# Performance work log

Hardware: AMD Instinct MI355X
Metric: run time of the kernel (lower is better)

## Reference

```python
import jax, jax.numpy as jnp
import numpy as np

B, V, E = 1024, 50257, 128

def setup_inputs() -> dict:
    key = jax.random.key(0)
    k1, k2, k3, k4 = jax.random.split(key, 4)
    # xs: one-hot focus-word vectors [B, V]
    focus_ids = jax.random.randint(k1, (B,), 0, V)
    xs = jnp.zeros((B, V), dtype=jnp.float32).at[jnp.arange(B), focus_ids].set(1.0)
    metric = jax.random.normal(k2, (E, E), dtype=jnp.float32)
    EMBEDM = jax.random.normal(k3, (V, E), dtype=jnp.float32)
    NEGEMBEDM = jax.random.normal(k4, (V, E), dtype=jnp.float32)
    return {"xs": xs, "metric": metric, "EMBEDM": EMBEDM, "NEGEMBEDM": NEGEMBEDM}

def reference(xs, metric, EMBEDM, NEGEMBEDM):
    # xs @ EMBEDM : one-hot matmul == row gather, but kept as GEMM to match original math
    xsembeds = xs @ EMBEDM                              # [B, E]
    # dots(vs, ws, metric) = (vs @ metric) @ ws.T
    scores = (xsembeds @ metric) @ NEGEMBEDM.T          # [B, V]
    return jax.nn.log_softmax(scores, axis=1)
```

## Files before the change

kernel.cpp:

```cpp
#include <hip/hip_runtime.h>
#include <hip/hip_bf16.h>
#include <math.h>

#define B_ROWS 1024
#define V_COLS 50257
#define E_DIM  128
#define BM     128
#define BN     128
#define NNB    393
#define VPAD   (NNB * BN)
#define N4     (V_COLS * E_DIM / 4)
#define N4P    (VPAD * E_DIM / 4)

typedef __attribute__((ext_vector_type(8))) short short8;
typedef __attribute__((ext_vector_type(4))) float floatx4;

static __device__ __forceinline__ unsigned short f2bf(float x) {
    union { float f; unsigned int u; } c; c.f = x;
    unsigned int u = c.u;
    unsigned int r = u + 0x7fffu + ((u >> 16) & 1u);
    return (unsigned short)(r >> 16);
}

static __device__ __forceinline__ void gload16(const void* g, void* l) {
    __builtin_amdgcn_global_load_lds(
        (const __attribute__((address_space(1))) void*)g,
        (__attribute__((address_space(3))) void*)l,
        16, 0, 0);
}

__global__ void find_idx_kernel(const float* __restrict__ xs, int* __restrict__ idx) {
    long i = (long)blockIdx.x * blockDim.x + threadIdx.x;
    const long n4 = (long)B_ROWS * V_COLS / 4;
    if (i >= n4) return;
    floatx4 v = __builtin_nontemporal_load((const floatx4*)xs + i);
    float vals[4] = {v.x, v.y, v.z, v.w};
    #pragma unroll
    for (int c = 0; c < 4; ++c) {
        if (vals[c] != 0.0f) {
            long f = 4 * i + c;
            int b = (int)(f / V_COLS);
            idx[b] = (int)(f - (long)b * V_COLS);
        }
    }
}

__global__ void cvt_bf16_kernel(const float* __restrict__ src, ushort4* __restrict__ dst) {
    int i = blockIdx.x * blockDim.x + threadIdx.x;
    if (i >= N4P) return;
    ushort4 o;
    if (i < N4) {
        floatx4 v = __builtin_nontemporal_load((const floatx4*)src + i);
        o.x = f2bf(v.x); o.y = f2bf(v.y); o.z = f2bf(v.z); o.w = f2bf(v.w);
    } else {
        o.x = 0; o.y = 0; o.z = 0; o.w = 0;
    }
    dst[i] = o;
}

__global__ void compute_t_kernel(const float* __restrict__ EMB, const float* __restrict__ metric,
                                 const int* __restrict__ idx, unsigned short* __restrict__ t) {
    __shared__ float erow[E_DIM];
    int b = blockIdx.x, tid = threadIdx.x;
    int id = idx[b];
    erow[tid] = EMB[(long)id * E_DIM + tid];
    __syncthreads();
    float acc = 0.f;
    #pragma unroll 16
    for (int k = 0; k < E_DIM; ++k) acc += erow[k] * metric[k * E_DIM + tid];
    t[b * E_DIM + tid] = f2bf(acc);
}

template <bool WRITE_OUT>
__global__ __launch_bounds__(512, 4) void gemm_kernel(const unsigned short* __restrict__ t,
                                                      const unsigned short* __restrict__ neg,
                                                      float2* __restrict__ partials,
                                                      const float* __restrict__ lse,
                                                      float* __restrict__ out) {
    __shared__ __align__(16) unsigned char smem[128 * 132 * 4];
    __shared__ float2 stats[4][128];
    __shared__ float lsev[128];

    const int tid  = threadIdx.x;
    const int lane = tid & 63, wave = tid >> 6;
    const int l16  = lane & 15, q = lane >> 4;
    const int wm   = wave >> 2, wn = wave & 3;
    const int mbase = blockIdx.x * BM;
    const int nbase = blockIdx.y * BN;

    if (WRITE_OUT && tid < 128) lsev[tid] = lse[mbase + tid];

    uint4* ldsA = (uint4*)smem;
    uint4* ldsB = (uint4*)(smem + 32768);
    const uint4* srcA = (const uint4*)(t + (size_t)mbase * E_DIM);
    const uint4* srcB = (const uint4*)(neg + (size_t)nbase * E_DIM);
    {
        const int p0 = wave * 256 + lane;
        #pragma unroll
        for (int i = 0; i < 4; ++i) {
            int p = p0 + i * 64;
            int r = p >> 4, c = p & 15;
            int s = (r << 4) + (c ^ (r & 15));
            int pbase = wave * 256 + i * 64;
            gload16(srcA + s, ldsA + pbase);
            gload16(srcB + s, ldsB + pbase);
        }
    }
    __syncthreads();

    floatx4 acc[4][2];
    #pragma unroll
    for (int i = 0; i < 4; ++i)
        #pragma unroll
        for (int j = 0; j < 2; ++j) acc[i][j] = (floatx4){0, 0, 0, 0};

    #pragma unroll
    for (int ks = 0; ks < 4; ++ks) {
        short8 af[4], bfr[2];
        #pragma unroll
        for (int mf = 0; mf < 4; ++mf) {
            int row = wm * 64 + mf * 16 + l16;
            af[mf] = *(const short8*)&ldsA[(row << 4) + ((ks * 4 + q) ^ (row & 15))];
        }
        #pragma unroll
        for (int nf = 0; nf < 2; ++nf) {
            int row = wn * 32 + nf * 16 + l16;
            bfr[nf] = *(const short8*)&ldsB[(row << 4) + ((ks * 4 + q) ^ (row & 15))];
        }
        #pragma unroll
        for (int mf = 0; mf < 4; ++mf)
            #pragma unroll
            for (int nf = 0; nf < 2; ++nf)
                acc[mf][nf] = __builtin_amdgcn_mfma_f32_16x16x32_bf16(af[mf], bfr[nf], acc[mf][nf], 0, 0, 0);
    }


    if (!WRITE_OUT) {
        const bool v0 = (nbase + wn * 32 + l16) < V_COLS;
        const bool v1 = (nbase + wn * 32 + 16 + l16) < V_COLS;
        #pragma unroll
        for (int mf = 0; mf < 4; ++mf) {
            #pragma unroll
            for (int r = 0; r < 4; ++r) {
                float mx = -INFINITY;
                if (v0) mx = acc[mf][0][r];
                if (v1) mx = fmaxf(mx, acc[mf][1][r]);
                #pragma unroll
                for (int d = 1; d < 16; d <<= 1) mx = fmaxf(mx, __shfl_xor(mx, d, 16));
                float s = 0.f;
                if (v0) s += __expf(acc[mf][0][r] - mx);
                if (v1) s += __expf(acc[mf][1][r] - mx);
                #pragma unroll
                for (int d = 1; d < 16; d <<= 1) s += __shfl_xor(s, d, 16);
                if (l16 == 0) stats[wn][wm * 64 + mf * 16 + q * 4 + r] = make_float2(mx, s);
            }
        }
        __syncthreads();
        if (tid < 128) {
            float2 p0 = stats[0][tid], p1 = stats[1][tid], p2 = stats[2][tid], p3 = stats[3][tid];
            float mm = fmaxf(fmaxf(p0.x, p1.x), fmaxf(p2.x, p3.x));
            float ss = p0.y * __expf(p0.x - mm) + p1.y * __expf(p1.x - mm)
                     + p2.y * __expf(p2.x - mm) + p3.y * __expf(p3.x - mm);
            partials[(long)(mbase + tid) * NNB + blockIdx.y] = make_float2(mm, ss);
        }
    } else {
        __syncthreads();
        float* sbuf = (float*)smem;
        #pragma unroll
        for (int mf = 0; mf < 4; ++mf)
            #pragma unroll
            for (int nf = 0; nf < 2; ++nf)
                #pragma unroll
                for (int r = 0; r < 4; ++r)
                    sbuf[(wm * 64 + mf * 16 + q * 4 + r) * 132 + wn * 32 + nf * 16 + l16] = acc[mf][nf][r];
        __syncthreads();
        #pragma unroll 4
        for (int it = 0; it < 32; ++it) {
            int i = it * 512 + tid;
            int r = i >> 7, c = i & 127;
            int col = nbase + c;
            if (col < V_COLS)
                __builtin_nontemporal_store(sbuf[r * 132 + c] - lsev[r],
                                            &out[(size_t)(mbase + r) * V_COLS + col]);
        }
    }
}

__global__ void merge_lse_kernel(const float2* __restrict__ partials, float* __restrict__ lse) {
    int b = blockIdx.x;
    int tid = threadIdx.x;
    float m = -INFINITY, s = 0.f;
    for (int i = tid; i < NNB; i += 256) {
        float2 p = partials[(long)b * NNB + i];
        if (p.x > m) { s = s * __expf(m - p.x) + p.y; m = p.x; }
        else         { s += p.y * __expf(p.x - m); }
    }
    __shared__ float sm[256], ss[256];
    sm[tid] = m; ss[tid] = s;
    __syncthreads();
    for (int off = 128; off > 0; off >>= 1) {
        if (tid < off) {
            float m1 = sm[tid], s1 = ss[tid];
            float m2 = sm[tid + off], s2 = ss[tid + off];
            float mm = fmaxf(m1, m2);
            sm[tid] = mm;
            ss[tid] = s1 * __expf(m1 - mm) + s2 * __expf(m2 - mm);
        }
        __syncthreads();
    }
    if (tid == 0) lse[b] = sm[0] + __logf(ss[0]);
}

extern "C" void kernel_launch(void* const* d_in, const int* in_sizes, int n_in,
                              void* d_out, int out_size, void* d_ws, size_t ws_size,
                              hipStream_t stream) {
    const float* xs     = (const float*)d_in[0];
    const float* metric = (const float*)d_in[1];
    const float* EMB    = (const float*)d_in[2];
    const float* NEG    = (const float*)d_in[3];
    float* out = (float*)d_out;

    char* ws = (char*)d_ws;
    int*            idx      = (int*)ws;
    unsigned short* t        = (unsigned short*)(ws + 4096);
    unsigned short* neg16    = (unsigned short*)(ws + 266240);
    float2*         partials = (float2*)(ws + 13144064);
    float*          lse      = (float*)(ws + 16363520);

    {
        long n4 = (long)B_ROWS * V_COLS / 4;
        int blocks = (int)((n4 + 255) / 256);
        find_idx_kernel<<<blocks, 256, 0, stream>>>(xs, idx);
    }
    cvt_bf16_kernel<<<(N4P + 255) / 256, 256, 0, stream>>>(NEG, (ushort4*)neg16);
    compute_t_kernel<<<B_ROWS, E_DIM, 0, stream>>>(EMB, metric, idx, t);
    gemm_kernel<false><<<dim3(B_ROWS / BM, NNB), 512, 0, stream>>>(t, neg16, partials, nullptr, nullptr);
    merge_lse_kernel<<<B_ROWS, 256, 0, stream>>>(partials, lse);
    gemm_kernel<true><<<dim3(B_ROWS / BM, NNB), 512, 0, stream>>>(t, neg16, partials, lse, out);
}
```

Before: 474.2 us.

## Fuse GEMM passes into one score write with an in-place LSE subtract

Replaces the two-pass GEMM (one pass for softmax stats, one recomputing scores to write the normalized output) with a single pass. That pass writes raw scores to the output and emits per-tile max/sum partials. A new merge kernel combines the partials into the row log-sum-exp and subtracts it in place from the output using vectorized read-modify-write. This removes the recomputed GEMM and a launch. In exchange, the full B×V output is read and written a second time, and the nontemporal store hint is dropped.

```diff
diff --git a/kernel.cpp b/kernel.cpp
--- a/kernel.cpp
+++ b/kernel.cpp
@@ -71,15 +71,12 @@
     t[b * E_DIM + tid] = f2bf(acc);
 }
 
-template <bool WRITE_OUT>
-__global__ __launch_bounds__(512, 4) void gemm_kernel(const unsigned short* __restrict__ t,
-                                                      const unsigned short* __restrict__ neg,
-                                                      float2* __restrict__ partials,
-                                                      const float* __restrict__ lse,
-                                                      float* __restrict__ out) {
+__global__ __launch_bounds__(512, 4) void gemm_score_kernel(const unsigned short* __restrict__ t,
+                                                            const unsigned short* __restrict__ neg,
+                                                            float2* __restrict__ partials,
+                                                            float* __restrict__ out) {
     __shared__ __align__(16) unsigned char smem[128 * 132 * 4];
     __shared__ float2 stats[4][128];
-    __shared__ float lsev[128];
 
     const int tid  = threadIdx.x;
     const int lane = tid & 63, wave = tid >> 6;
@@ -87,8 +84,6 @@
     const int wm   = wave >> 2, wn = wave & 3;
     const int mbase = blockIdx.x * BM;
     const int nbase = blockIdx.y * BN;
-
-    if (WRITE_OUT && tid < 128) lsev[tid] = lse[mbase + tid];
 
     uint4* ldsA = (uint4*)smem;
     uint4* ldsB = (uint4*)(smem + 32768);
@@ -135,70 +130,68 @@
     }
 
 
-    if (!WRITE_OUT) {
-        const bool v0 = (nbase + wn * 32 + l16) < V_COLS;
-        const bool v1 = (nbase + wn * 32 + 16 + l16) < V_COLS;
-        #pragma unroll
-        for (int mf = 0; mf < 4; ++mf) {
-            #pragma unroll
-            for (int r = 0; r < 4; ++r) {
-                float mx = -INFINITY;
-                if (v0) mx = acc[mf][0][r];
-                if (v1) mx = fmaxf(mx, acc[mf][1][r]);
-                #pragma unroll
-                for (int d = 1; d < 16; d <<= 1) mx = fmaxf(mx, __shfl_xor(mx, d, 16));
-                float s = 0.f;
-                if (v0) s += __expf(acc[mf][0][r] - mx);
-                if (v1) s += __expf(acc[mf][1][r] - mx);
-                #pragma unroll
-                for (int d = 1; d < 16; d <<= 1) s += __shfl_xor(s, d, 16);
-                if (l16 == 0) stats[wn][wm * 64 + mf * 16 + q * 4 + r] = make_float2(mx, s);
-            }
-        }
-        __syncthreads();
-        if (tid < 128) {
-            float2 p0 = stats[0][tid], p1 = stats[1][tid], p2 = stats[2][tid], p3 = stats[3][tid];
-            float mm = fmaxf(fmaxf(p0.x, p1.x), fmaxf(p2.x, p3.x));
-            float ss = p0.y * __expf(p0.x - mm) + p1.y * __expf(p1.x - mm)
-                     + p2.y * __expf(p2.x - mm) + p3.y * __expf(p3.x - mm);
-            partials[(long)(mbase + tid) * NNB + blockIdx.y] = make_float2(mm, ss);
-        }
-    } else {
-        __syncthreads();
-        float* sbuf = (float*)smem;
-        #pragma unroll
-        for (int mf = 0; mf < 4; ++mf)
-            #pragma unroll
-            for (int nf = 0; nf < 2; ++nf)
-                #pragma unroll
-                for (int r = 0; r < 4; ++r)
-                    sbuf[(wm * 64 + mf * 16 + q * 4 + r) * 132 + wn * 32 + nf * 16 + l16] = acc[mf][nf][r];
-        __syncthreads();
-        #pragma unroll 4
-        for (int it = 0; it < 32; ++it) {
-            int i = it * 512 + tid;
-            int r = i >> 7, c = i & 127;
-            int col = nbase + c;
-            if (col < V_COLS)
-                __builtin_nontemporal_store(sbuf[r * 132 + c] - lsev[r],
-                                            &out[(size_t)(mbase + r) * V_COLS + col]);
-        }
-    }
-}
-
-__global__ void merge_lse_kernel(const float2* __restrict__ partials, float* __restrict__ lse) {
+    const bool v0 = (nbase + wn * 32 + l16) < V_COLS;
+    const bool v1 = (nbase + wn * 32 + 16 + l16) < V_COLS;
+    #pragma unroll
+    for (int mf = 0; mf < 4; ++mf) {
+        #pragma unroll
+        for (int r = 0; r < 4; ++r) {
+            float mx = -INFINITY;
+            if (v0) mx = acc[mf][0][r];
+            if (v1) mx = fmaxf(mx, acc[mf][1][r]);
+            #pragma unroll
+            for (int d = 1; d < 16; d <<= 1) mx = fmaxf(mx, __shfl_xor(mx, d, 16));
+            float s = 0.f;
+            if (v0) s += __expf(acc[mf][0][r] - mx);
+            if (v1) s += __expf(acc[mf][1][r] - mx);
+            #pragma unroll
+            for (int d = 1; d < 16; d <<= 1) s += __shfl_xor(s, d, 16);
+            if (l16 == 0) stats[wn][wm * 64 + mf * 16 + q * 4 + r] = make_float2(mx, s);
+        }
+    }
+    __syncthreads();
+
+    if (tid < 128) {
+        float2 p0 = stats[0][tid], p1 = stats[1][tid], p2 = stats[2][tid], p3 = stats[3][tid];
+        float mm = fmaxf(fmaxf(p0.x, p1.x), fmaxf(p2.x, p3.x));
+        float ss = p0.y * __expf(p0.x - mm) + p1.y * __expf(p1.x - mm)
+                 + p2.y * __expf(p2.x - mm) + p3.y * __expf(p3.x - mm);
+        partials[(long)(mbase + tid) * NNB + blockIdx.y] = make_float2(mm, ss);
+    }
+
+    float* sbuf = (float*)smem;
+    #pragma unroll
+    for (int mf = 0; mf < 4; ++mf)
+        #pragma unroll
+        for (int nf = 0; nf < 2; ++nf)
+            #pragma unroll
+            for (int r = 0; r < 4; ++r)
+                sbuf[(wm * 64 + mf * 16 + q * 4 + r) * 132 + wn * 32 + nf * 16 + l16] = acc[mf][nf][r];
+    __syncthreads();
+    #pragma unroll 4
+    for (int it = 0; it < 32; ++it) {
+        int i = it * 512 + tid;
+        int r = i >> 7, c = i & 127;
+        int col = nbase + c;
+        if (col < V_COLS)
+            out[(size_t)(mbase + r) * V_COLS + col] = sbuf[r * 132 + c];
+    }
+}
+
+__global__ __launch_bounds__(512) void merge_sub_kernel(const float2* __restrict__ partials,
+                                                        float* __restrict__ out) {
     int b = blockIdx.x;
     int tid = threadIdx.x;
     float m = -INFINITY, s = 0.f;
-    for (int i = tid; i < NNB; i += 256) {
+    for (int i = tid; i < NNB; i += 512) {
         float2 p = partials[(long)b * NNB + i];
         if (p.x > m) { s = s * __expf(m - p.x) + p.y; m = p.x; }
         else         { s += p.y * __expf(p.x - m); }
     }
-    __shared__ float sm[256], ss[256];
+    __shared__ float sm[512], ss[512];
     sm[tid] = m; ss[tid] = s;
     __syncthreads();
-    for (int off = 128; off > 0; off >>= 1) {
+    for (int off = 256; off > 0; off >>= 1) {
         if (tid < off) {
             float m1 = sm[tid], s1 = ss[tid];
             float m2 = sm[tid + off], s2 = ss[tid + off];
@@ -208,7 +201,24 @@
         }
         __syncthreads();
     }
-    if (tid == 0) lse[b] = sm[0] + __logf(ss[0]);
+    __shared__ float lse_sh;
+    if (tid == 0) lse_sh = sm[0] + __logf(ss[0]);
+    __syncthreads();
+    const float l = lse_sh;
+
+    float* p = out + (size_t)b * V_COLS;
+    int mis  = (int)(((unsigned long long)(uintptr_t)p >> 2) & 3ull);
+    int head = (4 - mis) & 3;
+    if (tid < head) p[tid] -= l;
+    int n4 = (V_COLS - head) >> 2;
+    floatx4* p4 = (floatx4*)(p + head);
+    for (int i = tid; i < n4; i += 512) {
+        floatx4 v = p4[i];
+        v -= l;
+        p4[i] = v;
+    }
+    int done = head + (n4 << 2);
+    if (tid < V_COLS - done) p[done + tid] -= l;
 }
 
 extern "C" void kernel_launch(void* const* d_in, const int* in_sizes, int n_in,
@@ -225,7 +235,6 @@
     unsigned short* t        = (unsigned short*)(ws + 4096);
     unsigned short* neg16    = (unsigned short*)(ws + 266240);
     float2*         partials = (float2*)(ws + 13144064);
-    float*          lse      = (float*)(ws + 16363520);
 
     {
         long n4 = (long)B_ROWS * V_COLS / 4;
@@ -234,7 +243,6 @@
     }
     cvt_bf16_kernel<<<(N4P + 255) / 256, 256, 0, stream>>>(NEG, (ushort4*)neg16);
     compute_t_kernel<<<B_ROWS, E_DIM, 0, stream>>>(EMB, metric, idx, t);
-    gemm_kernel<false><<<dim3(B_ROWS / BM, NNB), 512, 0, stream>>>(t, neg16, partials, nullptr, nullptr);
-    merge_lse_kernel<<<B_ROWS, 256, 0, stream>>>(partials, lse);
-    gemm_kernel<true><<<dim3(B_ROWS / BM, NNB), 512, 0, stream>>>(t, neg16, partials, lse, out);
-}
+    gemm_score_kernel<<<dim3(B_ROWS / BM, NNB), 512, 0, stream>>>(t, neg16, partials, out);
+    merge_sub_kernel<<<B_ROWS, 512, 0, stream>>>(partials, out);
+}
```

Result: faster. 456.0 us (-3.8%).

## Make GEMM persistent over vocab chunks with double-buffered B tiles and online softmax

Applied to the files above, without the earlier changes.

The one-tile-per-block GEMM grid is replaced by 256 blocks, each owning a 128-row M tile and a contiguous chunk of about 12 vocab tiles. The A fragment stays in registers and B tiles are double-buffered in LDS with async global-to-LDS loads. The stats pass now keeps running max/sum per row in registers, and merge_lse shrinks to one 128-thread wave reduction. The write pass stores directly from registers instead of staging through LDS, which risks less-coalesced output stores and lower occupancy with only 256 blocks.

```diff
diff --git a/kernel.cpp b/kernel.cpp
--- a/kernel.cpp
+++ b/kernel.cpp
@@ -11,6 +11,7 @@
 #define VPAD   (NNB * BN)
 #define N4     (V_COLS * E_DIM / 4)
 #define N4P    (VPAD * E_DIM / 4)
+#define NCHUNK 32
 
 typedef __attribute__((ext_vector_type(8))) short short8;
 typedef __attribute__((ext_vector_type(4))) float floatx4;
@@ -72,143 +73,161 @@
 }
 
 template <bool WRITE_OUT>
-__global__ __launch_bounds__(512, 4) void gemm_kernel(const unsigned short* __restrict__ t,
-                                                      const unsigned short* __restrict__ neg,
-                                                      float2* __restrict__ partials,
-                                                      const float* __restrict__ lse,
-                                                      float* __restrict__ out) {
-    __shared__ __align__(16) unsigned char smem[128 * 132 * 4];
-    __shared__ float2 stats[4][128];
-    __shared__ float lsev[128];
+__global__ __launch_bounds__(512, 2) void gemm_chunk_kernel(const unsigned short* __restrict__ t,
+                                                            const unsigned short* __restrict__ neg,
+                                                            float2* __restrict__ partials,
+                                                            const float* __restrict__ lse,
+                                                            float* __restrict__ out) {
+    __shared__ __align__(16) uint4 bbuf[2][2048];
+
+    const int lin  = blockIdx.x;
+    const int m    = (lin >> 3) & 7;
+    const int c    = (lin & 7) | ((lin >> 6) << 3);
+    const int t0   = (c * NNB) / NCHUNK;
+    const int t1   = ((c + 1) * NNB) / NCHUNK;
 
     const int tid  = threadIdx.x;
     const int lane = tid & 63, wave = tid >> 6;
     const int l16  = lane & 15, q = lane >> 4;
     const int wm   = wave >> 2, wn = wave & 3;
-    const int mbase = blockIdx.x * BM;
-    const int nbase = blockIdx.y * BN;
-
-    if (WRITE_OUT && tid < 128) lsev[tid] = lse[mbase + tid];
-
-    uint4* ldsA = (uint4*)smem;
-    uint4* ldsB = (uint4*)(smem + 32768);
-    const uint4* srcA = (const uint4*)(t + (size_t)mbase * E_DIM);
-    const uint4* srcB = (const uint4*)(neg + (size_t)nbase * E_DIM);
-    {
-        const int p0 = wave * 256 + lane;
+    const int mbase = m * BM;
+
+    short8 af[4][4];
+    #pragma unroll
+    for (int mf = 0; mf < 4; ++mf)
+        #pragma unroll
+        for (int ks = 0; ks < 4; ++ks)
+            af[mf][ks] = *(const short8*)&t[(size_t)(mbase + wm * 64 + mf * 16 + l16) * E_DIM + ks * 32 + q * 8];
+
+    float lsev[4][4];
+    float mrun[4][4], srun[4][4];
+    if (WRITE_OUT) {
+        #pragma unroll
+        for (int mf = 0; mf < 4; ++mf)
+            #pragma unroll
+            for (int r = 0; r < 4; ++r)
+                lsev[mf][r] = lse[mbase + wm * 64 + mf * 16 + q * 4 + r];
+    } else {
+        #pragma unroll
+        for (int mf = 0; mf < 4; ++mf)
+            #pragma unroll
+            for (int r = 0; r < 4; ++r) { mrun[mf][r] = -INFINITY; srun[mf][r] = 0.f; }
+    }
+
+    const int p0 = wave * 256 + lane;
+    auto STAGE = [&](int buf, int tile) {
+        const uint4* srcB = (const uint4*)(neg + (size_t)tile * BN * E_DIM);
         #pragma unroll
         for (int i = 0; i < 4; ++i) {
             int p = p0 + i * 64;
-            int r = p >> 4, c = p & 15;
-            int s = (r << 4) + (c ^ (r & 15));
-            int pbase = wave * 256 + i * 64;
-            gload16(srcA + s, ldsA + pbase);
-            gload16(srcB + s, ldsB + pbase);
-        }
-    }
+            int r = p >> 4, cc = p & 15;
+            int s = (r << 4) + (cc ^ (r & 15));
+            gload16(srcB + s, &bbuf[buf][wave * 256 + i * 64]);
+        }
+    };
+
+    STAGE(0, t0);
     __syncthreads();
 
-    floatx4 acc[4][2];
+    for (int tt = t0; tt < t1; ++tt) {
+        const int cur = (tt - t0) & 1;
+        if (tt + 1 < t1) STAGE(cur ^ 1, tt + 1);
+
+        floatx4 acc[4][2];
+        #pragma unroll
+        for (int i = 0; i < 4; ++i)
+            #pragma unroll
+            for (int j = 0; j < 2; ++j) acc[i][j] = (floatx4){0, 0, 0, 0};
+
+        #pragma unroll
+        for (int ks = 0; ks < 4; ++ks) {
+            short8 bfr[2];
+            #pragma unroll
+            for (int nf = 0; nf < 2; ++nf) {
+                int row = wn * 32 + nf * 16 + l16;
+                bfr[nf] = *(const short8*)&bbuf[cur][(row << 4) + ((ks * 4 + q) ^ (row & 15))];
+            }
+            #pragma unroll
+            for (int mf = 0; mf < 4; ++mf)
+                #pragma unroll
+                for (int nf = 0; nf < 2; ++nf)
+                    acc[mf][nf] = __builtin_amdgcn_mfma_f32_16x16x32_bf16(af[mf][ks], bfr[nf], acc[mf][nf], 0, 0, 0);
+        }
+
+        const int col0 = tt * BN + wn * 32 + l16;
+        const bool v0 = col0 < V_COLS;
+        const bool v1 = (col0 + 16) < V_COLS;
+
+        if (!WRITE_OUT) {
+            #pragma unroll
+            for (int mf = 0; mf < 4; ++mf)
+                #pragma unroll
+                for (int r = 0; r < 4; ++r) {
+                    float a0 = v0 ? acc[mf][0][r] : -INFINITY;
+                    float a1 = v1 ? acc[mf][1][r] : -INFINITY;
+                    float nm = fmaxf(mrun[mf][r], fmaxf(a0, a1));
+                    float s  = srun[mf][r] * __expf(mrun[mf][r] - nm);
+                    if (v0) s += __expf(a0 - nm);
+                    if (v1) s += __expf(a1 - nm);
+                    mrun[mf][r] = nm; srun[mf][r] = s;
+                }
+        } else {
+            #pragma unroll
+            for (int mf = 0; mf < 4; ++mf) {
+                const size_t rowb = (size_t)(mbase + wm * 64 + mf * 16 + q * 4) * V_COLS;
+                #pragma unroll
+                for (int r = 0; r < 4; ++r) {
+                    if (v0) out[rowb + (size_t)r * V_COLS + col0]      = acc[mf][0][r] - lsev[mf][r];
+                    if (v1) out[rowb + (size_t)r * V_COLS + col0 + 16] = acc[mf][1][r] - lsev[mf][r];
+                }
+            }
+        }
+        __syncthreads();
+    }
+
+    if (!WRITE_OUT) {
+        #pragma unroll
+        for (int mf = 0; mf < 4; ++mf)
+            #pragma unroll
+            for (int r = 0; r < 4; ++r) {
+                float mm = mrun[mf][r], ss = srun[mf][r];
+                #pragma unroll
+                for (int d = 1; d < 16; d <<= 1) {
+                    float mo = __shfl_xor(mm, d, 16);
+                    float so = __shfl_xor(ss, d, 16);
+                    float nm = fmaxf(mm, mo);
+                    ss = ss * __expf(mm - nm) + so * __expf(mo - nm);
+                    mm = nm;
+                }
+                if (l16 == 0) {
+                    int row_local = wm * 64 + mf * 16 + q * 4 + r;
+                    partials[(((size_t)mbase + row_local) * NCHUNK + c) * 4 + wn] = make_float2(mm, ss);
+                }
+            }
+    }
+}
+
+__global__ __launch_bounds__(128) void merge_lse_kernel(const float2* __restrict__ partials,
+                                                        float* __restrict__ lse) {
+    int b = blockIdx.x, tid = threadIdx.x;
+    float2 p = partials[(size_t)b * 128 + tid];
+    float mm = p.x, ss = p.y;
     #pragma unroll
-    for (int i = 0; i < 4; ++i)
-        #pragma unroll
-        for (int j = 0; j < 2; ++j) acc[i][j] = (floatx4){0, 0, 0, 0};
-
-    #pragma unroll
-    for (int ks = 0; ks < 4; ++ks) {
-        short8 af[4], bfr[2];
-        #pragma unroll
-        for (int mf = 0; mf < 4; ++mf) {
-            int row = wm * 64 + mf * 16 + l16;
-            af[mf] = *(const short8*)&ldsA[(row << 4) + ((ks * 4 + q) ^ (row & 15))];
-        }
-        #pragma unroll
-        for (int nf = 0; nf < 2; ++nf) {
-            int row = wn * 32 + nf * 16 + l16;
-            bfr[nf] = *(const short8*)&ldsB[(row << 4) + ((ks * 4 + q) ^ (row & 15))];
-        }
-        #pragma unroll
-        for (int mf = 0; mf < 4; ++mf)
-            #pragma unroll
-            for (int nf = 0; nf < 2; ++nf)
-                acc[mf][nf] = __builtin_amdgcn_mfma_f32_16x16x32_bf16(af[mf], bfr[nf], acc[mf][nf], 0, 0, 0);
-    }
-
-
-    if (!WRITE_OUT) {
-        const bool v0 = (nbase + wn * 32 + l16) < V_COLS;
-        const bool v1 = (nbase + wn * 32 + 16 + l16) < V_COLS;
-        #pragma unroll
-        for (int mf = 0; mf < 4; ++mf) {
-            #pragma unroll
-            for (int r = 0; r < 4; ++r) {
-                float mx = -INFINITY;
-                if (v0) mx = acc[mf][0][r];
-                if (v1) mx = fmaxf(mx, acc[mf][1][r]);
-                #pragma unroll
-                for (int d = 1; d < 16; d <<= 1) mx = fmaxf(mx, __shfl_xor(mx, d, 16));
-                float s = 0.f;
-                if (v0) s += __expf(acc[mf][0][r] - mx);
-                if (v1) s += __expf(acc[mf][1][r] - mx);
-                #pragma unroll
-                for (int d = 1; d < 16; d <<= 1) s += __shfl_xor(s, d, 16);
-                if (l16 == 0) stats[wn][wm * 64 + mf * 16 + q * 4 + r] = make_float2(mx, s);
-            }
-        }
-        __syncthreads();
-        if (tid < 128) {
-            float2 p0 = stats[0][tid], p1 = stats[1][tid], p2 = stats[2][tid], p3 = stats[3][tid];
-            float mm = fmaxf(fmaxf(p0.x, p1.x), fmaxf(p2.x, p3.x));
-            float ss = p0.y * __expf(p0.x - mm) + p1.y * __expf(p1.x - mm)
-                     + p2.y * __expf(p2.x - mm) + p3.y * __expf(p3.x - mm);
-            partials[(long)(mbase + tid) * NNB + blockIdx.y] = make_float2(mm, ss);
-        }
-    } else {
-        __syncthreads();
-        float* sbuf = (float*)smem;
-        #pragma unroll
-        for (int mf = 0; mf < 4; ++mf)
-            #pragma unroll
-            for (int nf = 0; nf < 2; ++nf)
-                #pragma unroll
-                for (int r = 0; r < 4; ++r)
-                    sbuf[(wm * 64 + mf * 16 + q * 4 + r) * 132 + wn * 32 + nf * 16 + l16] = acc[mf][nf][r];
-        __syncthreads();
-        #pragma unroll 4
-        for (int it = 0; it < 32; ++it) {
-            int i = it * 512 + tid;
-            int r = i >> 7, c = i & 127;
-            int col = nbase + c;
-            if (col < V_COLS)
-                __builtin_nontemporal_store(sbuf[r * 132 + c] - lsev[r],
-                                            &out[(size_t)(mbase + r) * V_COLS + col]);
-        }
-    }
-}
-
-__global__ void merge_lse_kernel(const float2* __restrict__ partials, float* __restrict__ lse) {
-    int b = blockIdx.x;
-    int tid = threadIdx.x;
-    float m = -INFINITY, s = 0.f;
-    for (int i = tid; i < NNB; i += 256) {
-        float2 p = partials[(long)b * NNB + i];
-        if (p.x > m) { s = s * __expf(m - p.x) + p.y; m = p.x; }
-        else         { s += p.y * __expf(p.x - m); }
-    }
-    __shared__ float sm[256], ss[256];
-    sm[tid] = m; ss[tid] = s;
+    for (int d = 1; d < 64; d <<= 1) {
+        float mo = __shfl_xor(mm, d, 64);
+        float so = __shfl_xor(ss, d, 64);
+        float nm = fmaxf(mm, mo);
+        ss = ss * __expf(mm - nm) + so * __expf(mo - nm);
+        mm = nm;
+    }
+    __shared__ float m2[2], s2[2];
+    if ((tid & 63) == 0) { m2[tid >> 6] = mm; s2[tid >> 6] = ss; }
     __syncthreads();
-    for (int off = 128; off > 0; off >>= 1) {
-        if (tid < off) {
-            float m1 = sm[tid], s1 = ss[tid];
-            float m2 = sm[tid + off], s2 = ss[tid + off];
-            float mm = fmaxf(m1, m2);
-            sm[tid] = mm;
-            ss[tid] = s1 * __expf(m1 - mm) + s2 * __expf(m2 - mm);
-        }
-        __syncthreads();
-    }
-    if (tid == 0) lse[b] = sm[0] + __logf(ss[0]);
+    if (tid == 0) {
+        float nm = fmaxf(m2[0], m2[1]);
+        float s  = s2[0] * __expf(m2[0] - nm) + s2[1] * __expf(m2[1] - nm);
+        lse[b] = nm + __logf(s);
+    }
 }
 
 extern "C" void kernel_launch(void* const* d_in, const int* in_sizes, int n_in,
@@ -225,7 +244,7 @@
     unsigned short* t        = (unsigned short*)(ws + 4096);
     unsigned short* neg16    = (unsigned short*)(ws + 266240);
     float2*         partials = (float2*)(ws + 13144064);
-    float*          lse      = (float*)(ws + 16363520);
+    float*          lse      = (float*)(ws + 14192640);
 
     {
         long n4 = (long)B_ROWS * V_COLS / 4;
@@ -234,7 +253,7 @@
     }
     cvt_bf16_kernel<<<(N4P + 255) / 256, 256, 0, stream>>>(NEG, (ushort4*)neg16);
     compute_t_kernel<<<B_ROWS, E_DIM, 0, stream>>>(EMB, metric, idx, t);
-    gemm_kernel<false><<<dim3(B_ROWS / BM, NNB), 512, 0, stream>>>(t, neg16, partials, nullptr, nullptr);
-    merge_lse_kernel<<<B_ROWS, 256, 0, stream>>>(partials, lse);
-    gemm_kernel<true><<<dim3(B_ROWS / BM, NNB), 512, 0, stream>>>(t, neg16, partials, lse, out);
-}
+    gemm_chunk_kernel<false><<<8 * NCHUNK, 512, 0, stream>>>(t, neg16, partials, nullptr, nullptr);
+    merge_lse_kernel<<<B_ROWS, 128, 0, stream>>>(partials, lse);
+    gemm_chunk_kernel<true><<<8 * NCHUNK, 512, 0, stream>>>(t, neg16, partials, lse, out);
+}
```

Measured after the change: 438.5 us. 7.5% less time.
